# Performance work log

Hardware: AMD Instinct MI355X
Metric: run time of the kernel (lower is better)

## Reference

```python
import jax, jax.numpy as jnp
import numpy as np

N_NODES = 40000
N_EDGES = 640000
IN_CH = 128
HID_CH = 128
BN_EPS = 1e-5


def setup_inputs() -> dict:
    key = jax.random.key(0)
    k_x, k_ei, k_w, k_g = jax.random.split(key, 4)
    x = jax.random.normal(k_x, (N_NODES, IN_CH), dtype=jnp.float32)
    edge_index = jax.random.randint(k_ei, (2, N_EDGES), 0, N_NODES, dtype=jnp.int32)
    # Glorot init for GCNConv weight, zero bias (PyG defaults)
    limit = float(np.sqrt(6.0 / (IN_CH + HID_CH)))
    W = jax.random.uniform(k_w, (IN_CH, HID_CH), dtype=jnp.float32, minval=-limit, maxval=limit)
    b = jnp.zeros((HID_CH,), dtype=jnp.float32)
    gamma = jnp.ones((HID_CH,), dtype=jnp.float32)
    beta = jnp.zeros((HID_CH,), dtype=jnp.float32)
    return {"x": x, "edge_index": edge_index, "W": W, "b": b, "gamma": gamma, "beta": beta}


def reference(x, edge_index, W, b, gamma, beta):
    N = x.shape[0]
    src, dst = edge_index[0], edge_index[1]

    # --- GCNConv: h = x @ W, symmetric-normalized aggregation with self-loops ---
    h = x @ W  # [N, H]
    ones = jnp.ones((src.shape[0],), dtype=x.dtype)
    deg = jax.ops.segment_sum(ones, dst, num_segments=N) + 1.0  # +1 for self-loop
    dinv = jax.lax.rsqrt(deg)  # deg >= 1 always
    norm = dinv[src] * dinv[dst]  # [E]
    msg = h[src] * norm[:, None]  # [E, H] gather
    agg = jax.ops.segment_sum(msg, dst, num_segments=N)  # scatter-add
    agg = agg + h * (dinv * dinv)[:, None]  # self-loop contribution
    out = agg + b  # bias added after aggregation (PyG GCNConv)

    # --- BatchNorm1d (training mode: batch stats, biased variance) ---
    mean = jnp.mean(out, axis=0)
    var = jnp.mean((out - mean) ** 2, axis=0)
    out = gamma * (out - mean) * jax.lax.rsqrt(var + BN_EPS) + beta

    # --- ReLU (dropout is a no-op in eval) ---
    return jax.nn.relu(out)
```

## Files before the change

### kernel.cpp

```cpp
#include <hip/hip_runtime.h>

#define N_NODES 40000
#define N_EDGES 640000
#define CH 128
#define BN_EPS 1e-5f
#define CAP 48
#define CNT_S 8
#define MM_ROWS 32
#define MM_BLOCKS (N_NODES / MM_ROWS)
#define FILL_BLOCKS (N_EDGES / 512)
#define ZROW 40000


typedef __bf16 bf16x8 __attribute__((ext_vector_type(8)));
typedef float f32x4 __attribute__((ext_vector_type(4)));

__device__ __forceinline__ float bf_lo(unsigned u) { return __uint_as_float(u << 16); }
__device__ __forceinline__ float bf_hi(unsigned u) { return __uint_as_float(u & 0xffff0000u); }
__device__ __forceinline__ unsigned short f2bf(float f) {
    unsigned u = __float_as_uint(f);
    unsigned r = 0x7fffu + ((u >> 16) & 1u);
    return (unsigned short)((u + r) >> 16);
}
__device__ __forceinline__ unsigned pack2bf(float a, float b) {
    return (unsigned)f2bf(a) | ((unsigned)f2bf(b) << 16);
}

__global__ __launch_bounds__(256) void fill_kernel(const int* __restrict__ src,
                                                   const int* __restrict__ dst,
                                                   int* __restrict__ cnt,
                                                   unsigned short* __restrict__ bucket16,
                                                   unsigned* __restrict__ hbf_u32) {
    int t = threadIdx.x;
    int bb = blockIdx.x;
    if (bb == 0 && t < 64) hbf_u32[(size_t)ZROW * 64 + t] = 0u;
    int base = cnt[N_NODES * CNT_S];
    int i0 = bb * 512 + t;
    int i1 = i0 + 256;
    int d0 = dst[i0], d1 = dst[i1];
    int s0 = src[i0], s1 = src[i1];
    int sl0 = atomicAdd(&cnt[d0 * CNT_S], 1) - base;
    int sl1 = atomicAdd(&cnt[d1 * CNT_S], 1) - base;
    if (sl0 < CAP) bucket16[d0 * CAP + sl0] = (unsigned short)s0;
    if (sl1 < CAP) bucket16[d1 * CAP + sl1] = (unsigned short)s1;
}

__global__ __launch_bounds__(256) void mm_kernel(const float* __restrict__ x,
                                                 const float* __restrict__ W,
                                                 const int* __restrict__ cnt,
                                                 unsigned short* __restrict__ hbf) {
    __shared__ unsigned xl[MM_ROWS * 68];
    __shared__ float dinv_l[MM_ROWS];
    int t = threadIdx.x;
    int bb = blockIdx.x;
    size_t row0 = (size_t)bb * MM_ROWS;
    if (t < MM_ROWS) {
        int base = cnt[N_NODES * CNT_S];
        int c = cnt[(row0 + t) * CNT_S] - base;
        dinv_l[t] = rsqrtf((float)c + 1.0f);
    }
#pragma unroll
    for (int it = 0; it < MM_ROWS * 32 / 256; ++it) {
        int idx = it * 256 + t;
        int row = idx >> 5, c4 = idx & 31;
        float4 f = ((const float4*)(x + (row0 + row) * CH))[c4];
        uint2 p;
        p.x = pack2bf(f.x, f.y);
        p.y = pack2bf(f.z, f.w);
        *(uint2*)&xl[row * 68 + 2 * c4] = p;
    }
    int w = t >> 6, l = t & 63;
    int q = l >> 4, c15 = l & 15;
    int ct0 = 2 * w, ct1 = 2 * w + 1;
    bf16x8 bf0[4], bf1[4];
#pragma unroll
    for (int ks = 0; ks < 4; ++ks) {
        const float* wp = W + (size_t)(ks * 32 + 8 * q) * CH + c15;
        float v0[8], v1[8];
#pragma unroll
        for (int j = 0; j < 8; ++j) {
            v0[j] = wp[j * CH + ct0 * 16];
            v1[j] = wp[j * CH + ct1 * 16];
        }
        uint4 u0, u1;
        u0.x = pack2bf(v0[0], v0[1]); u0.y = pack2bf(v0[2], v0[3]);
        u0.z = pack2bf(v0[4], v0[5]); u0.w = pack2bf(v0[6], v0[7]);
        u1.x = pack2bf(v1[0], v1[1]); u1.y = pack2bf(v1[2], v1[3]);
        u1.z = pack2bf(v1[4], v1[5]); u1.w = pack2bf(v1[6], v1[7]);
        bf0[ks] = __builtin_bit_cast(bf16x8, u0);
        bf1[ks] = __builtin_bit_cast(bf16x8, u1);
    }
    __syncthreads();
#pragma unroll
    for (int rt = 0; rt < MM_ROWS / 16; ++rt) {
        int rbase = rt * 16 + c15;
        f32x4 acc0 = {0.f, 0.f, 0.f, 0.f};
        f32x4 acc1 = {0.f, 0.f, 0.f, 0.f};
#pragma unroll
        for (int ks = 0; ks < 4; ++ks) {
            uint4 ua = *(const uint4*)&xl[rbase * 68 + ks * 16 + 4 * q];
            bf16x8 af = __builtin_bit_cast(bf16x8, ua);
            acc0 = __builtin_amdgcn_mfma_f32_16x16x32_bf16(af, bf0[ks], acc0, 0, 0, 0);
            acc1 = __builtin_amdgcn_mfma_f32_16x16x32_bf16(af, bf1[ks], acc1, 0, 0, 0);
        }
        unsigned short* hr = hbf + (row0 + rt * 16 + q * 4) * CH;
#pragma unroll
        for (int r = 0; r < 4; ++r) {
            float dv = dinv_l[rt * 16 + q * 4 + r];
            hr[r * CH + ct0 * 16 + c15] = f2bf(acc0[r] * dv);
            hr[r * CH + ct1 * 16 + c15] = f2bf(acc1[r] * dv);
        }
    }
}

__global__ __launch_bounds__(256) void aggregate_kernel(const unsigned short* __restrict__ bucket16,
                                                        const int* __restrict__ cnt,
                                                        const unsigned* __restrict__ hbf_u32,
                                                        const float* __restrict__ b,
                                                        float* __restrict__ out,
                                                        float* __restrict__ sums32) {
    __shared__ float bsum[CH], bsq[CH];
    int t = threadIdx.x;
    if (t < CH) { bsum[t] = 0.0f; bsq[t] = 0.0f; }
    __syncthreads();
    int base = cnt[N_NODES * CNT_S];
    int wid = t >> 6;
    int lane = t & 63;
    int n_base = blockIdx.x * 16 + wid * 4;
    float2 bv = ((const float2*)b)[lane];

    int cn[4];
    unsigned bp[4], us[4];
#pragma unroll
    for (int it = 0; it < 4; ++it) cn[it] = cnt[(n_base + it) * CNT_S] - base;
#pragma unroll
    for (int it = 0; it < 4; ++it) bp[it] = (unsigned)bucket16[(n_base + it) * CAP + lane];
#pragma unroll
    for (int it = 0; it < 4; ++it) us[it] = hbf_u32[(size_t)(n_base + it) * 64 + lane];

    float slo = 0.f, shi = 0.f, qlo = 0.f, qhi = 0.f;
#pragma unroll
    for (int it = 0; it < 4; ++it) {
        int n = n_base + it;
        int m = cn[it] < CAP ? cn[it] : CAP;
        float dn = rsqrtf((float)cn[it] + 1.0f);
        unsigned sp = (lane < m) ? bp[it] : (unsigned)ZROW;
        float alo = bf_lo(us[it]);
        float ahi = bf_hi(us[it]);
        for (int jj = 0; jj < m; jj += 16) {
            unsigned u[16];
#pragma unroll
            for (int r = 0; r < 16; ++r) {
                unsigned sx = (unsigned)__shfl((int)sp, jj + r, 64);
                u[r] = hbf_u32[(size_t)sx * 64 + lane];
            }
#pragma unroll
            for (int r = 0; r < 16; ++r) {
                alo += bf_lo(u[r]);
                ahi += bf_hi(u[r]);
            }
        }
        float olo = alo * dn + bv.x;
        float ohi = ahi * dn + bv.y;
        float2 ov = {olo, ohi};
        *(float2*)(out + (size_t)n * CH + 2 * lane) = ov;
        slo += olo; qlo += olo * olo;
        shi += ohi; qhi += ohi * ohi;
    }
    atomicAdd(&bsum[2 * lane], slo);
    atomicAdd(&bsum[2 * lane + 1], shi);
    atomicAdd(&bsq[2 * lane], qlo);
    atomicAdd(&bsq[2 * lane + 1], qhi);
    __syncthreads();
    atomicAdd(&sums32[(blockIdx.x & 31) * 256 + t], (t < CH) ? bsum[t] : bsq[t - CH]);
}

__global__ __launch_bounds__(256) void bn_relu_kernel(float* __restrict__ out,
                                                      const float* __restrict__ sums32,
                                                      const float* __restrict__ gamma,
                                                      const float* __restrict__ beta) {
    __shared__ float sc[CH], sh[CH];
    int t = threadIdx.x;
    if (t < CH) {
        float P = sums32[32 * 256];
        float s = -32.0f * P, q = -32.0f * P;
#pragma unroll
        for (int k = 0; k < 32; ++k) {
            s += sums32[k * 256 + t];
            q += sums32[k * 256 + CH + t];
        }
        const float invN = 1.0f / (float)N_NODES;
        float mean = s * invN;
        float var = q * invN - mean * mean;
        float scale = gamma[t] * rsqrtf(var + BN_EPS);
        sc[t] = scale;
        sh[t] = beta[t] - mean * scale;
    }
    __syncthreads();
    int i = blockIdx.x * 256 + t;
    int c0 = (i & 31) * 4;
    float4 v = ((float4*)out)[i];
    float r0 = v.x * sc[c0] + sh[c0];
    float r1 = v.y * sc[c0 + 1] + sh[c0 + 1];
    float r2 = v.z * sc[c0 + 2] + sh[c0 + 2];
    float r3 = v.w * sc[c0 + 3] + sh[c0 + 3];
    v.x = r0 > 0.0f ? r0 : 0.0f;
    v.y = r1 > 0.0f ? r1 : 0.0f;
    v.z = r2 > 0.0f ? r2 : 0.0f;
    v.w = r3 > 0.0f ? r3 : 0.0f;
    ((float4*)out)[i] = v;
}

extern "C" void kernel_launch(void* const* d_in, const int* in_sizes, int n_in,
                              void* d_out, int out_size, void* d_ws, size_t ws_size,
                              hipStream_t stream) {
    const float* x = (const float*)d_in[0];
    const int* ei = (const int*)d_in[1];
    const float* W = (const float*)d_in[2];
    const float* b = (const float*)d_in[3];
    const float* gamma = (const float*)d_in[4];
    const float* beta = (const float*)d_in[5];
    float* out = (float*)d_out;
    const int* src = ei;
    const int* dst = ei + N_EDGES;
    char* ws = (char*)d_ws;

    unsigned short* hbf = (unsigned short*)ws;
    int* cnt = (int*)(ws + 10240256);
    float* sums32 = (float*)(ws + 11520512);
    unsigned short* bucket16 = (unsigned short*)(ws + 11553536);

    fill_kernel<<<FILL_BLOCKS, 256, 0, stream>>>(src, dst, cnt, bucket16, (unsigned*)hbf);
    mm_kernel<<<MM_BLOCKS, 256, 0, stream>>>(x, W, cnt, hbf);
    aggregate_kernel<<<N_NODES / 16, 256, 0, stream>>>(bucket16, cnt, (const unsigned*)hbf,
                                                       b, out, sums32);
    bn_relu_kernel<<<N_NODES * CH / 4 / 256, 256, 0, stream>>>(out, sums32, gamma, beta);
}
```

Baseline: 161.9 us.

## Gather neighbor rows with 16-byte loads split across wave quarters

The aggregation kernel now lets each quarter-wave fetch a whole bf16 neighbor row with uint4 loads, so one wave gathers four rows per instruction. Partial sums are combined with cross-quarter shuffles. Loads for the four nodes are issued in 16-neighbor stages before they are consumed, which puts more memory requests in flight. The cost is more registers, extra shuffle reductions, and more shared-memory atomics per thread for the BN statistics.

```diff
diff --git a/kernel.cpp b/kernel.cpp
--- a/kernel.cpp
+++ b/kernel.cpp
@@ -115,7 +115,7 @@
 
 __global__ __launch_bounds__(256) void aggregate_kernel(const unsigned short* __restrict__ bucket16,
                                                         const int* __restrict__ cnt,
-                                                        const unsigned* __restrict__ hbf_u32,
+                                                        const uint4* __restrict__ h4,
                                                         const float* __restrict__ b,
                                                         float* __restrict__ out,
                                                         float* __restrict__ sums32) {
@@ -126,53 +126,125 @@
     int base = cnt[N_NODES * CNT_S];
     int wid = t >> 6;
     int lane = t & 63;
-    int n_base = blockIdx.x * 16 + wid * 4;
-    float2 bv = ((const float2*)b)[lane];
-
-    int cn[4];
-    unsigned bp[4], us[4];
-#pragma unroll
-    for (int it = 0; it < 4; ++it) cn[it] = cnt[(n_base + it) * CNT_S] - base;
-#pragma unroll
-    for (int it = 0; it < 4; ++it) bp[it] = (unsigned)bucket16[(n_base + it) * CAP + lane];
-#pragma unroll
-    for (int it = 0; it < 4; ++it) us[it] = hbf_u32[(size_t)(n_base + it) * 64 + lane];
-
-    float slo = 0.f, shi = 0.f, qlo = 0.f, qhi = 0.f;
-#pragma unroll
-    for (int it = 0; it < 4; ++it) {
-        int n = n_base + it;
-        int m = cn[it] < CAP ? cn[it] : CAP;
-        float dn = rsqrtf((float)cn[it] + 1.0f);
-        unsigned sp = (lane < m) ? bp[it] : (unsigned)ZROW;
-        float alo = bf_lo(us[it]);
-        float ahi = bf_hi(us[it]);
-        for (int jj = 0; jj < m; jj += 16) {
-            unsigned u[16];
-#pragma unroll
-            for (int r = 0; r < 16; ++r) {
-                unsigned sx = (unsigned)__shfl((int)sp, jj + r, 64);
-                u[r] = hbf_u32[(size_t)sx * 64 + lane];
-            }
-#pragma unroll
-            for (int r = 0; r < 16; ++r) {
-                alo += bf_lo(u[r]);
-                ahi += bf_hi(u[r]);
-            }
-        }
-        float olo = alo * dn + bv.x;
-        float ohi = ahi * dn + bv.y;
-        float2 ov = {olo, ohi};
-        *(float2*)(out + (size_t)n * CH + 2 * lane) = ov;
-        slo += olo; qlo += olo * olo;
-        shi += ohi; qhi += ohi * ohi;
-    }
-    atomicAdd(&bsum[2 * lane], slo);
-    atomicAdd(&bsum[2 * lane + 1], shi);
-    atomicAdd(&bsq[2 * lane], qlo);
-    atomicAdd(&bsq[2 * lane + 1], qhi);
+    int quarter = lane >> 4;
+    int ql = lane & 15;
+    int n0 = blockIdx.x * 16 + wid * 4;
+
+    int cn0 = cnt[(n0 + 0) * CNT_S] - base;
+    int cn1 = cnt[(n0 + 1) * CNT_S] - base;
+    int cn2 = cnt[(n0 + 2) * CNT_S] - base;
+    int cn3 = cnt[(n0 + 3) * CNT_S] - base;
+    unsigned sp0 = (unsigned)bucket16[(n0 + 0) * CAP + lane];
+    unsigned sp1 = (unsigned)bucket16[(n0 + 1) * CAP + lane];
+    unsigned sp2 = (unsigned)bucket16[(n0 + 2) * CAP + lane];
+    unsigned sp3 = (unsigned)bucket16[(n0 + 3) * CAP + lane];
+    int m0 = cn0 < CAP ? cn0 : CAP;
+    int m1 = cn1 < CAP ? cn1 : CAP;
+    int m2 = cn2 < CAP ? cn2 : CAP;
+    int m3 = cn3 < CAP ? cn3 : CAP;
+    sp0 = (lane < m0) ? sp0 : (unsigned)ZROW;
+    sp1 = (lane < m1) ? sp1 : (unsigned)ZROW;
+    sp2 = (lane < m2) ? sp2 : (unsigned)ZROW;
+    sp3 = (lane < m3) ? sp3 : (unsigned)ZROW;
+    float dn0 = rsqrtf((float)cn0 + 1.0f);
+    float dn1 = rsqrtf((float)cn1 + 1.0f);
+    float dn2 = rsqrtf((float)cn2 + 1.0f);
+    float dn3 = rsqrtf((float)cn3 + 1.0f);
+
+    float a0[8] = {0, 0, 0, 0, 0, 0, 0, 0};
+    float a1[8] = {0, 0, 0, 0, 0, 0, 0, 0};
+    float a2[8] = {0, 0, 0, 0, 0, 0, 0, 0};
+    float a3[8] = {0, 0, 0, 0, 0, 0, 0, 0};
+
+#define ISSUE(u, sp, bs)                                                     \
+    {                                                                        \
+        int sxa = __shfl((int)(sp), (bs) + 0 + quarter, 64);                 \
+        int sxb = __shfl((int)(sp), (bs) + 4 + quarter, 64);                 \
+        int sxc = __shfl((int)(sp), (bs) + 8 + quarter, 64);                 \
+        int sxd = __shfl((int)(sp), (bs) + 12 + quarter, 64);                \
+        u[0] = h4[(size_t)(unsigned)sxa * 16 + ql];                          \
+        u[1] = h4[(size_t)(unsigned)sxb * 16 + ql];                          \
+        u[2] = h4[(size_t)(unsigned)sxc * 16 + ql];                          \
+        u[3] = h4[(size_t)(unsigned)sxd * 16 + ql];                          \
+    }
+#define CONSUME(u, a)                                                        \
+    _Pragma("unroll") for (int r = 0; r < 4; ++r) {                          \
+        a[0] += bf_lo(u[r].x); a[1] += bf_hi(u[r].x);                        \
+        a[2] += bf_lo(u[r].y); a[3] += bf_hi(u[r].y);                        \
+        a[4] += bf_lo(u[r].z); a[5] += bf_hi(u[r].z);                        \
+        a[6] += bf_lo(u[r].w); a[7] += bf_hi(u[r].w);                        \
+    }
+
+    uint4 u0[4], u1[4], u2[4], u3[4];
+    if (m0 > 0) ISSUE(u0, sp0, 0);
+    if (m1 > 0) ISSUE(u1, sp1, 0);
+    if (m2 > 0) ISSUE(u2, sp2, 0);
+    if (m3 > 0) ISSUE(u3, sp3, 0);
+    if (m0 > 0) CONSUME(u0, a0);
+    if (m1 > 0) CONSUME(u1, a1);
+    if (m2 > 0) CONSUME(u2, a2);
+    if (m3 > 0) CONSUME(u3, a3);
+    if (m0 > 16) ISSUE(u0, sp0, 16);
+    if (m1 > 16) ISSUE(u1, sp1, 16);
+    if (m2 > 16) ISSUE(u2, sp2, 16);
+    if (m3 > 16) ISSUE(u3, sp3, 16);
+    if (m0 > 16) CONSUME(u0, a0);
+    if (m1 > 16) CONSUME(u1, a1);
+    if (m2 > 16) CONSUME(u2, a2);
+    if (m3 > 16) CONSUME(u3, a3);
+    if (m0 > 32) ISSUE(u0, sp0, 32);
+    if (m1 > 32) ISSUE(u1, sp1, 32);
+    if (m2 > 32) ISSUE(u2, sp2, 32);
+    if (m3 > 32) ISSUE(u3, sp3, 32);
+    if (m0 > 32) CONSUME(u0, a0);
+    if (m1 > 32) CONSUME(u1, a1);
+    if (m2 > 32) CONSUME(u2, a2);
+    if (m3 > 32) CONSUME(u3, a3);
+
+#define RED(a)                                                               \
+    _Pragma("unroll") for (int k = 0; k < 8; ++k) {                          \
+        float v = a[k];                                                      \
+        v += __shfl_xor(v, 16, 64);                                          \
+        v += __shfl_xor(v, 32, 64);                                          \
+        a[k] = v;                                                            \
+    }
+    RED(a0) RED(a1) RED(a2) RED(a3)
+
+    uint4 sf = h4[(size_t)(n0 + quarter) * 16 + ql];
+    float4 bva = ((const float4*)b)[ql * 2];
+    float4 bvb = ((const float4*)b)[ql * 2 + 1];
+    float dnq = (quarter & 2) ? ((quarter & 1) ? dn3 : dn2)
+                              : ((quarter & 1) ? dn1 : dn0);
+    float o[8];
+#pragma unroll
+    for (int k = 0; k < 8; ++k) {
+        float v01 = (quarter & 1) ? a1[k] : a0[k];
+        float v23 = (quarter & 1) ? a3[k] : a2[k];
+        o[k] = (quarter & 2) ? v23 : v01;
+    }
+    o[0] = (o[0] + bf_lo(sf.x)) * dnq + bva.x;
+    o[1] = (o[1] + bf_hi(sf.x)) * dnq + bva.y;
+    o[2] = (o[2] + bf_lo(sf.y)) * dnq + bva.z;
+    o[3] = (o[3] + bf_hi(sf.y)) * dnq + bva.w;
+    o[4] = (o[4] + bf_lo(sf.z)) * dnq + bvb.x;
+    o[5] = (o[5] + bf_hi(sf.z)) * dnq + bvb.y;
+    o[6] = (o[6] + bf_lo(sf.w)) * dnq + bvb.z;
+    o[7] = (o[7] + bf_hi(sf.w)) * dnq + bvb.w;
+    float4* op = (float4*)(out + (size_t)(n0 + quarter) * CH + ql * 8);
+    float4 w0 = {o[0], o[1], o[2], o[3]};
+    float4 w1 = {o[4], o[5], o[6], o[7]};
+    op[0] = w0;
+    op[1] = w1;
+#pragma unroll
+    for (int k = 0; k < 8; ++k) {
+        atomicAdd(&bsum[ql * 8 + k], o[k]);
+        atomicAdd(&bsq[ql * 8 + k], o[k] * o[k]);
+    }
     __syncthreads();
     atomicAdd(&sums32[(blockIdx.x & 31) * 256 + t], (t < CH) ? bsum[t] : bsq[t - CH]);
+#undef ISSUE
+#undef CONSUME
+#undef RED
 }
 
 __global__ __launch_bounds__(256) void bn_relu_kernel(float* __restrict__ out,
@@ -232,7 +304,7 @@
 
     fill_kernel<<<FILL_BLOCKS, 256, 0, stream>>>(src, dst, cnt, bucket16, (unsigned*)hbf);
     mm_kernel<<<MM_BLOCKS, 256, 0, stream>>>(x, W, cnt, hbf);
-    aggregate_kernel<<<N_NODES / 16, 256, 0, stream>>>(bucket16, cnt, (const unsigned*)hbf,
+    aggregate_kernel<<<N_NODES / 16, 256, 0, stream>>>(bucket16, cnt, (const uint4*)hbf,
                                                        b, out, sums32);
     bn_relu_kernel<<<N_NODES * CH / 4 / 256, 256, 0, stream>>>(out, sums32, gamma, beta);
 }
```

New measurement: 201.0 us. 1.24x slower.
